# Optimization experiments

Measured on AMD Instinct MI355X. Metric: run time of the kernel, lower is better.

Reference implementation:

```python
import jax, jax.numpy as jnp
import numpy as np

D = H = W = 64
N = D * H * W
BS = 2
C = 32          # enc_dim
IN_DIM = 4
OUT_DIM = 4
P = 5           # pos_enc_dim
COND = 32
M = 8           # modes per axis
NL = 4          # n_layers
NODE_IN = IN_DIM + 3 + 2 * P * 3   # 37
ENC_T = 1 + 2 * P                  # 11
ENC_C = ENC_T * COND               # 352
DT = 0.05


def fourier_embedding(pos, n_freq):
    # F(x) = [cos(2^i*pi*x_l), sin(2^i*pi*x_l)] per coordinate l, then concat x
    freq = (2.0 ** jnp.arange(n_freq, dtype=jnp.float32)) * jnp.pi  # (P,)
    ang = pos[..., None] * freq                                     # (..., L, P)
    emb = jnp.concatenate([jnp.cos(ang), jnp.sin(ang)], axis=-1)    # (..., L, 2P)
    emb = emb.reshape(*pos.shape[:-1], -1)                          # (..., L*2P)
    return jnp.concatenate([emb, pos], axis=-1)


def setup_inputs() -> dict:
    key = jax.random.key(0)
    ks = jax.random.split(key, 24)
    scale = 1.0 / C ** 2
    inp = {
        "state_in": jax.random.normal(ks[0], (BS, N, IN_DIM), jnp.float32),
        "node_pos": jax.random.uniform(ks[1], (BS, N, 3), jnp.float32),
        "edges": jax.random.randint(ks[2], (BS, 16, 2), 0, N),
        "time_i": jax.random.uniform(ks[3], (BS, 1), jnp.float32),
        "conditions": jax.random.uniform(ks[4], (BS, COND), jnp.float32),
        "t_embed_w": jax.random.normal(ks[5], (C, ENC_T), jnp.float32) * 0.05,
        "t_embed_b": jax.random.normal(ks[6], (C,), jnp.float32) * 0.05,
        "c_embed_w": jax.random.normal(ks[7], (C, ENC_C), jnp.float32) * 0.05,
        "c_embed_b": jax.random.normal(ks[8], (C,), jnp.float32) * 0.05,
        "lift_w": jax.random.normal(ks[9], (C, NODE_IN), jnp.float32) * 0.05,
        "lift_b": jax.random.normal(ks[10], (C,), jnp.float32) * 0.05,
        "spec_wr": jax.random.uniform(ks[11], (NL, C, C, M, M, M), jnp.float32) * scale,
        "spec_wi": jax.random.uniform(ks[12], (NL, C, C, M, M, M), jnp.float32) * scale,
        "byp_w": jax.random.normal(ks[13], (NL, C, C), jnp.float32) * 0.05,
        "byp_b": jax.random.normal(ks[14], (NL, C), jnp.float32) * 0.05,
        "proj1_w": jax.random.normal(ks[15], (C, C), jnp.float32) * 0.05,
        "proj1_b": jax.random.normal(ks[16], (C,), jnp.float32) * 0.05,
        "proj2_w": jax.random.normal(ks[17], (OUT_DIM, C), jnp.float32) * 0.05,
        "proj2_b": jax.random.normal(ks[18], (OUT_DIM,), jnp.float32) * 0.05,
    }
    return inp


def _conv1x1(x, w, b):
    # x: (b, c, d, h, w), w: (o, c), b: (o,)
    return jnp.einsum('bcdhw,oc->bodhw', x, w) + b[None, :, None, None, None]


def _fno_forward(state_in, node_pos, time_i, conditions,
                 t_embed_w, t_embed_b, c_embed_w, c_embed_b, lift_w, lift_b,
                 spec_wr, spec_wi, byp_w, byp_b, proj1_w, proj1_b, proj2_w, proj2_b):
    pos_enc = fourier_embedding(node_pos, P)      # (bs, N, 33)
    c_enc = fourier_embedding(conditions, P)      # (bs, 352)
    t_enc = fourier_embedding(time_i, P)          # (bs, 11)

    node_feat = jnp.concatenate([state_in, pos_enc], axis=-1)  # (bs, N, 37)
    t_emb = (t_enc @ t_embed_w.T + t_embed_b)[:, :, None, None, None]
    c_emb = (c_enc @ c_embed_w.T + c_embed_b)[:, :, None, None, None]

    # (bs, N, 37) -> (bs, 37, D, H, W)
    x = node_feat.transpose(0, 2, 1).reshape(BS, NODE_IN, D, H, W)
    x = _conv1x1(x, lift_w, lift_b)
    x = x + t_emb + c_emb

    for l in range(NL):
        w = jax.lax.complex(spec_wr[l], spec_wi[l])              # (C, C, M, M, M)
        x_ft = jnp.fft.rfftn(x, axes=(-3, -2, -1))               # (bs, C, D, H, W//2+1)
        blk = jnp.einsum('bixyz,ioxyz->boxyz', x_ft[..., :M, :M, :M], w)
        out_ft = jnp.zeros_like(x_ft).at[..., :M, :M, :M].set(blk)
        sp = jnp.fft.irfftn(out_ft, s=(D, H, W), axes=(-3, -2, -1))
        bp = _conv1x1(x, byp_w[l], byp_b[l])
        x = jax.nn.gelu(sp + bp, approximate=False)

    x = jax.nn.gelu(_conv1x1(x, proj1_w, proj1_b), approximate=False)
    x = _conv1x1(x, proj2_w, proj2_b)                            # (bs, 4, D, H, W)
    v_pred = x.reshape(BS, OUT_DIM, N).transpose(0, 2, 1)        # (bs, N, 4)
    return state_in + DT * v_pred


def reference(state_in, node_pos, edges, time_i, conditions,
              t_embed_w, t_embed_b, c_embed_w, c_embed_b, lift_w, lift_b,
              spec_wr, spec_wi, byp_w, byp_b, proj1_w, proj1_b, proj2_w, proj2_b):
    # edges are unused in the FNO forward (kept for API compatibility)
    return _fno_forward(state_in, node_pos, time_i, conditions,
                        t_embed_w, t_embed_b, c_embed_w, c_embed_b, lift_w, lift_b,
                        spec_wr, spec_wi, byp_w, byp_b, proj1_w, proj1_b, proj2_w, proj2_b)
```

## Files before the change

### kernel.cpp

```cpp
#include <hip/hip_runtime.h>
#include <math.h>

#define PI_F 3.14159265358979323846f

typedef __bf16 bf16x8 __attribute__((ext_vector_type(8)));
typedef float floatx4 __attribute__((ext_vector_type(4)));
union U8 { unsigned short u[8]; uint4 q; bf16x8 v; };

__device__ __forceinline__ float gelu_sig(float v) {
    float e = __builtin_amdgcn_exp2f(-2.4554670f * v);
    return v * __builtin_amdgcn_rcpf(1.0f + e);
}
__device__ __forceinline__ int rfl(int x) { return __builtin_amdgcn_readfirstlane(x); }

__device__ __forceinline__ unsigned short f2bf(float f) {
    unsigned int u = __float_as_uint(f);
    u += 0x7fffu + ((u >> 16) & 1u);
    return (unsigned short)(u >> 16);
}
__device__ __forceinline__ float bf2f(unsigned short h) {
    return __uint_as_float(((unsigned int)h) << 16);
}

__device__ __forceinline__ void swz8k(int blk, int& b, int& nx, int& ny) {
    int x = blk & 7;
    int j = blk >> 3;
    int pair = x * 16 + (j >> 6);
    ny = j & 63;
    b = pair >> 6;
    nx = pair & 63;
}

__global__ void k_emb(const float* __restrict__ time_i, const float* __restrict__ conditions,
                      const float* __restrict__ t_embed_w, const float* __restrict__ t_embed_b,
                      const float* __restrict__ c_embed_w, const float* __restrict__ c_embed_b,
                      const float* __restrict__ lift_b, float* __restrict__ embk) {
    __shared__ float red[8][32];
    int t = threadIdx.x;
    int b = blockIdx.x;
    int c = t & 31, lg = t >> 5;
    float acc = 0.0f;
    if (lg == 0) {
        acc = t_embed_b[c] + c_embed_b[c] + lift_b[c];
        float tv = time_i[b];
        float ang = PI_F * tv;
        const float* tw = t_embed_w + c * 11;
        for (int i = 0; i < 5; i++) {
            float s, co; sincosf(ang, &s, &co);
            acc += co * tw[i] + s * tw[5 + i];
            ang *= 2.0f;
        }
        acc += tv * tw[10];
    }
    const float* cw = c_embed_w + c * 352;
    for (int j = 0; j < 4; j++) {
        int l = lg * 4 + j;
        float v = conditions[b * 32 + l];
        float ang = PI_F * v;
        for (int i = 0; i < 5; i++) {
            float s, co; sincosf(ang, &s, &co);
            acc += co * cw[l * 10 + i] + s * cw[l * 10 + 5 + i];
            ang *= 2.0f;
        }
        acc += v * cw[320 + l];
    }
    red[lg][c] = acc;
    __syncthreads();
    if (t < 32) {
        float s = 0.0f;
        for (int g = 0; g < 8; g++) s += red[g][t];
        embk[b * 32 + t] = s;
    }
}

__global__ void k_wt(const float* __restrict__ byp_w, const float* __restrict__ lift_w,
                     unsigned short* __restrict__ wbh, unsigned short* __restrict__ wlbf,
                     unsigned short* __restrict__ Tinv, unsigned short* __restrict__ TfT) {
    int idx = blockIdx.x * 256 + threadIdx.x;
    const float th = PI_F / 32.0f;
    if (idx < 4096) {
        wbh[idx] = f2bf(byp_w[idx]);
    } else if (idx < 6144) {
        int j = idx - 4096;
        int o = j >> 6, q = j & 63;
        wlbf[j] = (q < 37) ? f2bf(lift_w[o * 37 + q]) : 0;
    } else if (idx < 8192) {
        int j = idx - 6144;
        int nz = j >> 5, k = j & 31;
        int kz = k >> 1;
        float val = 0.0f;
        if (kz < 8) {
            float a = (float)((kz * nz) & 63) * th;
            val = (k & 1) ? sinf(a) : cosf(a);
        }
        Tinv[j] = f2bf(val);
    } else if (idx < 9216) {
        int j = idx - 8192;
        int kcol = j >> 6, nz = j & 63;
        int kz = kcol >> 1;
        float a = (float)((kz * nz) & 63) * th;
        float val = (kcol & 1) ? -sinf(a) : cosf(a);
        TfT[j] = f2bf(val);
    }
}

__global__ __launch_bounds__(256) void k_lift(const float* __restrict__ state_in,
        const float* __restrict__ node_pos, const unsigned short* __restrict__ wlbf,
        const float* __restrict__ embk, const unsigned short* __restrict__ TfT,
        unsigned short* __restrict__ x0, float2* __restrict__ a1) {
    __shared__ __align__(16) float SL[7584];
    unsigned short* fsT  = (unsigned short*)SL;
    unsigned short* ysbf = (unsigned short*)(SL + 2304);
    float* pz   = SL + 3456;
    float* pz2  = SL + 3456 + 512;
    float* bias = SL + 7552;
    int t = threadIdx.x;
    int b, nx, ny; swz8k(blockIdx.x, b, nx, ny);
    int nxy = nx * 64 + ny;

    if (t < 32) bias[t] = embk[b * 32 + t];
    {
        for (int u = t; u < 2048; u += 256) {
            int row = u >> 5, col = 37 + (u & 31);
            fsT[row * 72 + col] = 0;
        }
    }
    if (t < 192) {
        int nzf = t / 3;
        int l = t - nzf * 3;
        float p = node_pos[((size_t)b * 262144 + (nxy << 6)) * 3 + t];
        float s, c; sincosf(PI_F * p, &s, &c);
        unsigned short* row = fsT + nzf * 72;
        #pragma unroll
        for (int i = 0; i < 5; i++) {
            row[4 + l * 10 + i] = f2bf(c);
            row[4 + l * 10 + 5 + i] = f2bf(s);
            float nc = 2.0f * c * c - 1.0f;
            s = 2.0f * s * c;
            c = nc;
        }
        row[34 + l] = f2bf(p);
    } else {
        int nzf = t - 192;
        const float4 s4 = *(const float4*)(state_in + ((size_t)b * 262144 + (nxy << 6) + nzf) * 4);
        unsigned short* row = fsT + nzf * 72;
        row[0] = f2bf(s4.x); row[1] = f2bf(s4.y);
        row[2] = f2bf(s4.z); row[3] = f2bf(s4.w);
    }
    __syncthreads();

    int lane = t & 63;
    int w = rfl(t >> 6);
    int otile = w & 1;
    int nzt0 = (w >> 1) * 2;
    int l15 = lane & 15;
    int quad = lane >> 4;

    U8 a0, a1_;
    a0.q = *(const uint4*)(wlbf + ((otile * 16 + l15) << 6) + (quad << 3));
    a1_.q = *(const uint4*)(wlbf + ((otile * 16 + l15) << 6) + 32 + (quad << 3));
    floatx4 cb;
    #pragma unroll
    for (int r = 0; r < 4; r++) cb[r] = bias[otile * 16 + quad * 4 + r];
    floatx4 dz = {0.0f, 0.0f, 0.0f, 0.0f};

    #pragma unroll
    for (int m = 0; m < 2; m++) {
        int nzc = (nzt0 + m) * 16 + l15;
        U8 b0, b1_;
        b0.q = *(const uint4*)(fsT + nzc * 72 + (quad << 3));
        b1_.q = *(const uint4*)(fsT + nzc * 72 + 32 + (quad << 3));
        floatx4 d = __builtin_amdgcn_mfma_f32_16x16x32_bf16(a0.v, b0.v, cb, 0, 0, 0);
        d = __builtin_amdgcn_mfma_f32_16x16x32_bf16(a1_.v, b1_.v, d, 0, 0, 0);
        #pragma unroll
        for (int r = 0; r < 4; r++) {
            int o = otile * 16 + quad * 4 + r;
            ysbf[o * 72 + nzc] = f2bf(d[r]);
        }
    }
    __syncthreads();
    {
        int ch = t >> 3, q = t & 7;
        uint4 v = *(const uint4*)(ysbf + ch * 72 + q * 8);
        *(uint4*)(x0 + (((size_t)(b * 32 + ch)) << 18) + (nxy << 6) + q * 8) = v;
    }
    {
        int khalf = w >> 1;
        U8 ay, bt;
        ay.q = *(const uint4*)(ysbf + (otile * 16 + l15) * 72 + khalf * 32 + (quad << 3));
        bt.q = *(const uint4*)(TfT + (l15 << 6) + khalf * 32 + (quad << 3));
        floatx4 d = __builtin_amdgcn_mfma_f32_16x16x32_bf16(ay.v, bt.v, dz, 0, 0, 0);
        *(floatx4*)(pz + w * 1024 + lane * 4) = d;
    }
    __syncthreads();
    if (w < 2) {
        float4 p0 = *(float4*)(pz + w * 1024 + lane * 4);
        float4 p1 = *(float4*)(pz + (w + 2) * 1024 + lane * 4);
        float pv[4] = {p0.x + p1.x, p0.y + p1.y, p0.z + p1.z, p0.w + p1.w};
        #pragma unroll
        for (int r = 0; r < 4; r++)
            pz2[(otile * 16 + quad * 4 + r) * 16 + l15] = pv[r];
    }
    __syncthreads();
    if (t < 128) {
        float4 v = *(float4*)(pz2 + t * 4);
        float* a1f = (float*)a1 + ((size_t)(b * 4096 + nxy)) * 512;
        *(float4*)(a1f + t * 4) = v;
    }
}


__global__ __launch_bounds__(256) void k_p1(const float2* __restrict__ a1,
                                            float2* __restrict__ a2p) {
    int blk = blockIdx.x, t = threadIdx.x;
    int x = blk & 7, r = blk >> 3;
    int pair = x * 16 + (r & 15);
    int half = r >> 4;
    const float2* src = a1 + ((size_t)(pair * 64 + half * 32)) * 256 + t;
    float accr[8], acci[8];
    #pragma unroll
    for (int k = 0; k < 8; k++) { accr[k] = 0.0f; acci[k] = 0.0f; }
    const float bc = 0.99518472667f;
    const float bs = -0.09801714033f;
    float wc = half ? -1.0f : 1.0f;
    float ws = 0.0f;
    #pragma unroll 4
    for (int j = 0; j < 32; j++) {
        float2 v = src[(size_t)j * 256];
        accr[0] += v.x; acci[0] += v.y;
        float tc = wc, ts = ws;
        #pragma unroll
        for (int ky = 1; ky < 8; ky++) {
            accr[ky] += v.x * tc - v.y * ts;
            acci[ky] += v.x * ts + v.y * tc;
            float nt = tc * wc - ts * ws; ts = ts * wc + tc * ws; tc = nt;
        }
        float nw = wc * bc - ws * bs; ws = ws * bc + wc * bs; wc = nw;
    }
    float4* dst = (float4*)(a2p + (size_t)half * 262144 + ((size_t)(pair * 256 + t)) * 8);
    #pragma unroll
    for (int j = 0; j < 4; j++)
        dst[j] = make_float4(accr[2 * j], acci[2 * j], accr[2 * j + 1], acci[2 * j + 1]);
}

__global__ __launch_bounds__(256) void k_p2(const float2* __restrict__ a2p,
                                            float2* __restrict__ xft) {
    __shared__ __align__(16) float2 SH[1040];
    int blk = blockIdx.x, t = threadIdx.x;
    for (int lu = 0; lu < 2; lu++) {
        int un = blk * 2 + lu;
        int b = un >> 8, ckz = un & 255;
        size_t base = (size_t)b * 131072 + (size_t)ckz * 8;
        for (int e = t; e < 512; e += 256) {
            size_t a = base + (size_t)(e >> 3) * 2048 + (e & 7);
            float2 v0 = a2p[a];
            float2 v1 = a2p[a + 262144];
            SH[lu * 520 + e] = make_float2(v0.x + v1.x, v0.y + v1.y);
        }
    }
    __syncthreads();
    if (t < 128) {
        int lu = t >> 6, out = t & 63;
        int un = blk * 2 + lu;
        int kx = out & 7;
        float sn, cc; sincosf((float)kx * (PI_F / 32.0f), &sn, &cc);
        float bsn = -sn;
        float tc = 1.0f, ts = 0.0f, rr = 0.0f, ri = 0.0f;
        const float2* row = SH + lu * 520 + (out >> 3);
        for (int nx = 0; nx < 64; nx++) {
            float2 v = row[nx * 8];
            rr += v.x * tc - v.y * ts;
            ri += v.x * ts + v.y * tc;
            float nt = tc * cc - ts * bsn; ts = ts * cc + tc * bsn; tc = nt;
        }
        xft[(size_t)un * 64 + out] = make_float2(rr, ri);
    }
}

__global__ __launch_bounds__(256) void k_p3(const float2* __restrict__ xft,
        const float* __restrict__ wr, const float* __restrict__ wi,
        float2* __restrict__ yftp) {
    __shared__ __align__(16) float2 SH[128];
    int blk = blockIdx.x, t = threadIdx.x;
    int unit = blk >> 1, ih = blk & 1;
    int b = unit >> 6, kx = (unit >> 3) & 7, ky = unit & 7;
    if (t < 128) {
        int il = t >> 3, kz = t & 7;
        int i = ih * 16 + il;
        SH[t] = xft[((size_t)((b * 32 + i) * 8 + kz)) * 64 + ky * 8 + kx];
    }
    __syncthreads();
    int o = t >> 3, kz = t & 7;
    float yr = 0.0f, yi = 0.0f;
    for (int il = 0; il < 16; il++) {
        int i = ih * 16 + il;
        float2 xv = SH[il * 8 + kz];
        int wofs = ((i * 32 + o) << 9) + kx * 64 + ky * 8 + kz;
        float wrv = wr[wofs], wiv = wi[wofs];
        yr += xv.x * wrv - xv.y * wiv;
        yi += xv.x * wiv + xv.y * wrv;
    }
    yftp[(size_t)ih * 32768 + ((size_t)((b * 32 + o) * 8 + kz)) * 64 + ky * 8 + kx]
        = make_float2(yr, yi);
}

__global__ __launch_bounds__(256) void k_p4(const float2* __restrict__ yftp,
                                            float2* __restrict__ b1) {
    __shared__ __align__(16) float2 SH[4608];
    int blk = blockIdx.x, t = threadIdx.x;
    for (int u = 0; u < 2; u++) {
        if (u) __syncthreads();
        int unit = blk * 2 + u;
        int b = unit >> 8, nx = (unit >> 2) & 63, og = unit & 3;
        size_t sbase = ((size_t)(b * 32 + og * 8)) * 512;
        for (int e = t; e < 4096; e += 256) {
            float2 v0 = yftp[sbase + e];
            float2 v1 = yftp[32768 + sbase + e];
            SH[(e >> 3) * 9 + (e & 7)] = make_float2(v0.x + v1.x, v0.y + v1.y);
        }
        __syncthreads();
        float cs, ss; sincosf((float)nx * (PI_F / 32.0f), &ss, &cs);
        float2* dst = b1 + ((size_t)(b * 64 + nx)) * 2048 + og * 512;
        for (int h = 0; h < 2; h++) {
            int idx = h * 256 + t;
            const float2* row = SH + idx * 9;
            float c = 1.0f, s = 0.0f, rr = 0.0f, ri = 0.0f;
            #pragma unroll
            for (int kx = 0; kx < 8; kx++) {
                float2 y = row[kx];
                rr += y.x * c - y.y * s;
                ri += y.x * s + y.y * c;
                float nc = c * cs - s * ss; s = s * cs + c * ss; c = nc;
            }
            dst[idx] = make_float2(rr, ri);
        }
    }
}

__global__ __launch_bounds__(256) void k_fin(
        const unsigned short* __restrict__ xin, const float2* __restrict__ b1,
        const unsigned short* __restrict__ wbh, const float* __restrict__ bb,
        const unsigned short* __restrict__ Tinv, const unsigned short* __restrict__ TfT,
        unsigned short* __restrict__ xout, float2* __restrict__ a1, int do_z,
        int do_proj, const float* __restrict__ state_in, const float* __restrict__ p1w,
        const float* __restrict__ p1b, const float* __restrict__ p2w,
        const float* __restrict__ p2b, float* __restrict__ outp) {
    __shared__ __align__(16) float S[7232];
    float* b1sr = S;
    float* b1si = S + 2112;
    float* pz   = S;
    float* pz2  = S + 512;
    float* pr   = S;
    unsigned short* xsu  = (unsigned short*)(S + 4224);
    unsigned short* msbf = (unsigned short*)(S + 5280);
    unsigned short* ysbf = (unsigned short*)(S + 5920);
    float* cosT = S + 7072;
    float* sinT = S + 7136;
    float* bias = S + 7200;
    int t = threadIdx.x;
    int b, nx, ny; swz8k(blockIdx.x, b, nx, ny);
    int nxy = nx * 64 + ny;

    if (t < 64) { float s, c; sincosf((float)t * (PI_F / 32.0f), &s, &c); cosT[t] = c; sinT[t] = s; }
    if (t >= 96 && t < 128) bias[t - 96] = bb[t - 96];
    ((unsigned int*)msbf)[(t >> 3) * 20 + 8 + (t & 7)] = 0;
    {
        int ch = t >> 3, q = t & 7;
        uint4 v = *(const uint4*)(xin + (((size_t)b) << 23) + (nxy << 6)
                                  + ((size_t)ch << 18) + q * 8);
        unsigned int* dst = (unsigned int*)(xsu + ch * 66 + q * 8);
        dst[0] = v.x; dst[1] = v.y; dst[2] = v.z; dst[3] = v.w;
    }
    const float2* bsrc = b1 + ((size_t)(b * 64 + nx)) * 2048;
    for (int u = 0; u < 8; u++) {
        int g = u * 256 + t;
        float2 v = bsrc[g];
        int ky = g & 7, okz = g >> 3;
        b1sr[ky * 264 + okz] = v.x;
        b1si[ky * 264 + okz] = v.y;
    }
    __syncthreads();
    const float scale = 1.0f / 262144.0f;
    {
        float mr = 0.0f, mi = 0.0f;
        #pragma unroll
        for (int ky = 0; ky < 8; ky++) {
            float vr = b1sr[ky * 264 + t], vi = b1si[ky * 264 + t];
            int m_ = (ky * ny) & 63;
            float c = cosT[m_], s = sinT[m_];
            mr += vr * c - vi * s;
            mi += vr * s + vi * c;
        }
        int kz = t & 7;
        float sc = (kz == 0) ? scale : 2.0f * scale;
        unsigned int pk = (unsigned int)f2bf(mr * sc)
                        | ((unsigned int)f2bf(-mi * sc) << 16);
        ((unsigned int*)msbf)[(t >> 3) * 20 + kz] = pk;
    }
    __syncthreads();

    int lane = t & 63;
    int w = rfl(t >> 6);
    int otile = w & 1;
    int nzt0 = (w >> 1) * 2;
    int l15 = lane & 15;
    int quad = lane >> 4;

    U8 aw, ams;
    aw.q = *(const uint4*)(wbh + ((otile * 16 + l15) << 5) + (quad << 3));
    ams.q = *(const uint4*)(msbf + (otile * 16 + l15) * 40 + (quad << 3));
    floatx4 cb;
    #pragma unroll
    for (int r = 0; r < 4; r++) cb[r] = bias[otile * 16 + quad * 4 + r];
    floatx4 dzero = {0.0f, 0.0f, 0.0f, 0.0f};

    size_t colbase = (((size_t)b) << 23) + (nxy << 6);

    #pragma unroll
    for (int m = 0; m < 2; m++) {
        int nzc = (nzt0 + m) * 16 + l15;
        U8 bx, bt;
        #pragma unroll
        for (int j = 0; j < 8; j++) bx.u[j] = xsu[(quad * 8 + j) * 66 + nzc];
        bt.q = *(const uint4*)(Tinv + (nzc << 5) + (quad << 3));
        floatx4 d = __builtin_amdgcn_mfma_f32_16x16x32_bf16(aw.v, bx.v, cb, 0, 0, 0);
        d = __builtin_amdgcn_mfma_f32_16x16x32_bf16(ams.v, bt.v, d, 0, 0, 0);
        #pragma unroll
        for (int r = 0; r < 4; r++) {
            int o = otile * 16 + quad * 4 + r;
            ysbf[o * 72 + nzc] = f2bf(gelu_sig(d[r]));
        }
    }
    __syncthreads();

    if (!do_proj) {
        int ch = t >> 3, q = t & 7;
        uint4 v = *(const uint4*)(ysbf + ch * 72 + q * 8);
        *(uint4*)(xout + colbase + ((size_t)ch << 18) + q * 8) = v;
    }

    if (do_z) {
        int khalf = w >> 1;
        U8 ay, bt;
        ay.q = *(const uint4*)(ysbf + (otile * 16 + l15) * 72 + khalf * 32 + (quad << 3));
        bt.q = *(const uint4*)(TfT + (l15 << 6) + khalf * 32 + (quad << 3));
        floatx4 d = __builtin_amdgcn_mfma_f32_16x16x32_bf16(ay.v, bt.v, dzero, 0, 0, 0);
        *(floatx4*)(pz + w * 1024 + lane * 4) = d;
        __syncthreads();
        if (w < 2) {
            float4 p0 = *(float4*)(pz + w * 1024 + lane * 4);
            float4 p1 = *(float4*)(pz + (w + 2) * 1024 + lane * 4);
            float pv[4] = {p0.x + p1.x, p0.y + p1.y, p0.z + p1.z, p0.w + p1.w};
            #pragma unroll
            for (int r = 0; r < 4; r++)
                pz2[(otile * 16 + quad * 4 + r) * 16 + l15] = pv[r];
        }
        __syncthreads();
        if (t < 128) {
            float4 v = *(float4*)(pz2 + t * 4);
            float* a1f = (float*)a1 + ((size_t)(b * 4096 + nxy)) * 512;
            *(float4*)(a1f + t * 4) = v;
        }
    }

    if (do_proj) {
        int nz = t & 63;
        float xv[32];
        #pragma unroll
        for (int i = 0; i < 32; i++) xv[i] = bf2f(ysbf[i * 72 + nz]);
        float r0 = 0.f, r1 = 0.f, r2 = 0.f, r3 = 0.f;
        #pragma unroll
        for (int k = 0; k < 8; k++) {
            int o = w * 8 + k;
            float a = p1b[o];
            const float* wr = p1w + o * 32;
            #pragma unroll
            for (int i = 0; i < 32; i++) a += wr[i] * xv[i];
            float h = gelu_sig(a);
            r0 += p2w[0 * 32 + o] * h;
            r1 += p2w[1 * 32 + o] * h;
            r2 += p2w[2 * 32 + o] * h;
            r3 += p2w[3 * 32 + o] * h;
        }
        *(float4*)(pr + w * 256 + nz * 4) = make_float4(r0, r1, r2, r3);
        __syncthreads();
        if (t < 64) {
            float4 a0 = *(float4*)(pr + 0 * 256 + t * 4);
            float4 a1_ = *(float4*)(pr + 1 * 256 + t * 4);
            float4 a2 = *(float4*)(pr + 2 * 256 + t * 4);
            float4 a3 = *(float4*)(pr + 3 * 256 + t * 4);
            size_t base = ((size_t)b * 262144 + (nxy << 6) + t) * 4;
            float4 sv = *(const float4*)(state_in + base);
            *(float4*)(outp + base) = make_float4(
                sv.x + 0.05f * (p2b[0] + a0.x + a1_.x + a2.x + a3.x),
                sv.y + 0.05f * (p2b[1] + a0.y + a1_.y + a2.y + a3.y),
                sv.z + 0.05f * (p2b[2] + a0.z + a1_.z + a2.z + a3.z),
                sv.w + 0.05f * (p2b[3] + a0.w + a1_.w + a2.w + a3.w));
        }
    }
}

extern "C" void kernel_launch(void* const* d_in, const int* in_sizes, int n_in,
                              void* d_out, int out_size, void* d_ws, size_t ws_size,
                              hipStream_t stream) {
    const float* state_in   = (const float*)d_in[0];
    const float* node_pos   = (const float*)d_in[1];
    const float* time_i     = (const float*)d_in[3];
    const float* conditions = (const float*)d_in[4];
    const float* t_embed_w  = (const float*)d_in[5];
    const float* t_embed_b  = (const float*)d_in[6];
    const float* c_embed_w  = (const float*)d_in[7];
    const float* c_embed_b  = (const float*)d_in[8];
    const float* lift_w     = (const float*)d_in[9];
    const float* lift_b     = (const float*)d_in[10];
    const float* spec_wr    = (const float*)d_in[11];
    const float* spec_wi    = (const float*)d_in[12];
    const float* byp_w      = (const float*)d_in[13];
    const float* byp_b      = (const float*)d_in[14];
    const float* proj1_w    = (const float*)d_in[15];
    const float* proj1_b    = (const float*)d_in[16];
    const float* proj2_w    = (const float*)d_in[17];
    const float* proj2_b    = (const float*)d_in[18];
    float* out = (float*)d_out;
    float* ws  = (float*)d_ws;

    unsigned short* xA = (unsigned short*)ws;
    unsigned short* xB = (unsigned short*)(ws + 8388608);
    float2* a1   = (float2*)(ws + 16777216);
    float2* a2p  = (float2*)(ws + 20971520);
    float2* xft  = (float2*)(ws + 22020096);
    float2* yftp = (float2*)(ws + 22085632);
    float2* b1   = (float2*)(ws + 22216704);
    float*  embk = ws + 22740992;
    unsigned short* wbh  = (unsigned short*)(ws + 22741056);
    unsigned short* wlbf = (unsigned short*)(ws + 22743104);
    unsigned short* Tinv = (unsigned short*)(ws + 22744128);
    unsigned short* TfT  = (unsigned short*)(ws + 22745152);

    k_emb<<<2, 256, 0, stream>>>(time_i, conditions, t_embed_w, t_embed_b,
                                 c_embed_w, c_embed_b, lift_b, embk);
    k_wt<<<36, 256, 0, stream>>>(byp_w, lift_w, wbh, wlbf, Tinv, TfT);
    k_lift<<<8192, 256, 0, stream>>>(state_in, node_pos, wlbf, embk, TfT, xA, a1);

    for (int l = 0; l < 4; l++) {
        unsigned short* xin  = (l & 1) ? xB : xA;
        unsigned short* xout = (l & 1) ? xA : xB;
        const float* wrl = spec_wr + (size_t)l * 524288;
        const float* wil = spec_wi + (size_t)l * 524288;
        k_p1<<<256, 256, 0, stream>>>(a1, a2p);
        k_p2<<<256, 256, 0, stream>>>(a2p, xft);
        k_p3<<<256, 256, 0, stream>>>(xft, wrl, wil, yftp);
        k_p4<<<256, 256, 0, stream>>>(yftp, b1);
        k_fin<<<8192, 256, 0, stream>>>(xin, b1, wbh + l * 1024, byp_b + l * 32,
                                        Tinv, TfT, xout, a1, (l < 3) ? 1 : 0,
                                        (l == 3) ? 1 : 0, state_in,
                                        proj1_w, proj1_b, proj2_w, proj2_b, out);
    }
}
```

Measured before the change: 360.6 us.

## Split spectral partial sums four ways and process two columns per fin block

k_p1 and k_p3 now split their reductions into quarters instead of halves, doubling grid size to 512 blocks, with the partial sums added in k_p2 and k_p4. k_p1 and k_fin read precomputed ky*ny twiddles from a global table instead of rotating twiddles recursively or reading per-block LDS tables. k_fin handles two (nx,ny) columns per block, which halves the grid, and each wave now does a full 64-length z-transform MFMA pair rather than reducing partials through shared memory. The aim is more parallelism in the small spectral kernels and less per-block overhead in fin, at the cost of extra partial-buffer traffic and more LDS per block.

```diff
diff --git a/kernel.cpp b/kernel.cpp
--- a/kernel.cpp
+++ b/kernel.cpp
@@ -20,15 +20,6 @@
 }
 __device__ __forceinline__ float bf2f(unsigned short h) {
     return __uint_as_float(((unsigned int)h) << 16);
-}
-
-__device__ __forceinline__ void swz8k(int blk, int& b, int& nx, int& ny) {
-    int x = blk & 7;
-    int j = blk >> 3;
-    int pair = x * 16 + (j >> 6);
-    ny = j & 63;
-    b = pair >> 6;
-    nx = pair & 63;
 }
 
 __global__ void k_emb(const float* __restrict__ time_i, const float* __restrict__ conditions,
@@ -75,7 +66,8 @@
 
 __global__ void k_wt(const float* __restrict__ byp_w, const float* __restrict__ lift_w,
                      unsigned short* __restrict__ wbh, unsigned short* __restrict__ wlbf,
-                     unsigned short* __restrict__ Tinv, unsigned short* __restrict__ TfT) {
+                     unsigned short* __restrict__ Tinv, unsigned short* __restrict__ TfT,
+                     float* __restrict__ Tp1g) {
     int idx = blockIdx.x * 256 + threadIdx.x;
     const float th = PI_F / 32.0f;
     if (idx < 4096) {
@@ -101,7 +93,22 @@
         float a = (float)((kz * nz) & 63) * th;
         float val = (kcol & 1) ? -sinf(a) : cosf(a);
         TfT[j] = f2bf(val);
-    }
+    } else if (idx < 9728) {
+        int j = idx - 9216;
+        int ny = j >> 3, ky = j & 7;
+        float a = (float)((ky * ny) & 63) * th;
+        Tp1g[j * 2] = cosf(a);
+        Tp1g[j * 2 + 1] = sinf(a);
+    }
+}
+
+__device__ __forceinline__ void swz8k(int blk, int& b, int& nx, int& ny) {
+    int x = blk & 7;
+    int j = blk >> 3;
+    int pair = x * 16 + (j >> 6);
+    ny = j & 63;
+    b = pair >> 6;
+    nx = pair & 63;
 }
 
 __global__ __launch_bounds__(256) void k_lift(const float* __restrict__ state_in,
@@ -211,33 +218,28 @@
 
 
 __global__ __launch_bounds__(256) void k_p1(const float2* __restrict__ a1,
-                                            float2* __restrict__ a2p) {
+        const float2* __restrict__ Tp1g, float2* __restrict__ a2p) {
     int blk = blockIdx.x, t = threadIdx.x;
     int x = blk & 7, r = blk >> 3;
     int pair = x * 16 + (r & 15);
-    int half = r >> 4;
-    const float2* src = a1 + ((size_t)(pair * 64 + half * 32)) * 256 + t;
+    int qtr = r >> 4;
+    const float2* src = a1 + ((size_t)(pair * 64 + qtr * 16)) * 256 + t;
     float accr[8], acci[8];
     #pragma unroll
     for (int k = 0; k < 8; k++) { accr[k] = 0.0f; acci[k] = 0.0f; }
-    const float bc = 0.99518472667f;
-    const float bs = -0.09801714033f;
-    float wc = half ? -1.0f : 1.0f;
-    float ws = 0.0f;
     #pragma unroll 4
-    for (int j = 0; j < 32; j++) {
+    for (int j = 0; j < 16; j++) {
+        int ny = qtr * 16 + j;
         float2 v = src[(size_t)j * 256];
-        accr[0] += v.x; acci[0] += v.y;
-        float tc = wc, ts = ws;
-        #pragma unroll
-        for (int ky = 1; ky < 8; ky++) {
-            accr[ky] += v.x * tc - v.y * ts;
-            acci[ky] += v.x * ts + v.y * tc;
-            float nt = tc * wc - ts * ws; ts = ts * wc + tc * ws; tc = nt;
-        }
-        float nw = wc * bc - ws * bs; ws = ws * bc + wc * bs; wc = nw;
-    }
-    float4* dst = (float4*)(a2p + (size_t)half * 262144 + ((size_t)(pair * 256 + t)) * 8);
+        const float2* tw = Tp1g + ny * 8;
+        #pragma unroll
+        for (int ky = 0; ky < 8; ky++) {
+            float2 w2 = tw[ky];
+            accr[ky] += v.x * w2.x + v.y * w2.y;
+            acci[ky] += v.y * w2.x - v.x * w2.y;
+        }
+    }
+    float4* dst = (float4*)(a2p + (size_t)qtr * 262144 + ((size_t)(pair * 256 + t)) * 8);
     #pragma unroll
     for (int j = 0; j < 4; j++)
         dst[j] = make_float4(accr[2 * j], acci[2 * j], accr[2 * j + 1], acci[2 * j + 1]);
@@ -255,7 +257,10 @@
             size_t a = base + (size_t)(e >> 3) * 2048 + (e & 7);
             float2 v0 = a2p[a];
             float2 v1 = a2p[a + 262144];
-            SH[lu * 520 + e] = make_float2(v0.x + v1.x, v0.y + v1.y);
+            float2 v2 = a2p[a + 524288];
+            float2 v3 = a2p[a + 786432];
+            SH[lu * 520 + e] = make_float2(v0.x + v1.x + v2.x + v3.x,
+                                           v0.y + v1.y + v2.y + v3.y);
         }
     }
     __syncthreads();
@@ -280,27 +285,27 @@
 __global__ __launch_bounds__(256) void k_p3(const float2* __restrict__ xft,
         const float* __restrict__ wr, const float* __restrict__ wi,
         float2* __restrict__ yftp) {
-    __shared__ __align__(16) float2 SH[128];
+    __shared__ __align__(16) float2 SH[64];
     int blk = blockIdx.x, t = threadIdx.x;
-    int unit = blk >> 1, ih = blk & 1;
+    int unit = blk >> 2, iq = blk & 3;
     int b = unit >> 6, kx = (unit >> 3) & 7, ky = unit & 7;
-    if (t < 128) {
+    if (t < 64) {
         int il = t >> 3, kz = t & 7;
-        int i = ih * 16 + il;
+        int i = iq * 8 + il;
         SH[t] = xft[((size_t)((b * 32 + i) * 8 + kz)) * 64 + ky * 8 + kx];
     }
     __syncthreads();
     int o = t >> 3, kz = t & 7;
     float yr = 0.0f, yi = 0.0f;
-    for (int il = 0; il < 16; il++) {
-        int i = ih * 16 + il;
+    for (int il = 0; il < 8; il++) {
+        int i = iq * 8 + il;
         float2 xv = SH[il * 8 + kz];
         int wofs = ((i * 32 + o) << 9) + kx * 64 + ky * 8 + kz;
         float wrv = wr[wofs], wiv = wi[wofs];
         yr += xv.x * wrv - xv.y * wiv;
         yi += xv.x * wiv + xv.y * wrv;
     }
-    yftp[(size_t)ih * 32768 + ((size_t)((b * 32 + o) * 8 + kz)) * 64 + ky * 8 + kx]
+    yftp[(size_t)iq * 32768 + ((size_t)((b * 32 + o) * 8 + kz)) * 64 + ky * 8 + kx]
         = make_float2(yr, yi);
 }
 
@@ -316,7 +321,10 @@
         for (int e = t; e < 4096; e += 256) {
             float2 v0 = yftp[sbase + e];
             float2 v1 = yftp[32768 + sbase + e];
-            SH[(e >> 3) * 9 + (e & 7)] = make_float2(v0.x + v1.x, v0.y + v1.y);
+            float2 v2 = yftp[65536 + sbase + e];
+            float2 v3 = yftp[98304 + sbase + e];
+            SH[(e >> 3) * 9 + (e & 7)] = make_float2(v0.x + v1.x + v2.x + v3.x,
+                                                     v0.y + v1.y + v2.y + v3.y);
         }
         __syncthreads();
         float cs, ss; sincosf((float)nx * (PI_F / 32.0f), &ss, &cs);
@@ -341,35 +349,40 @@
         const unsigned short* __restrict__ xin, const float2* __restrict__ b1,
         const unsigned short* __restrict__ wbh, const float* __restrict__ bb,
         const unsigned short* __restrict__ Tinv, const unsigned short* __restrict__ TfT,
-        unsigned short* __restrict__ xout, float2* __restrict__ a1, int do_z,
-        int do_proj, const float* __restrict__ state_in, const float* __restrict__ p1w,
+        const float2* __restrict__ Tp1g, unsigned short* __restrict__ xout,
+        float2* __restrict__ a1, int do_z, int do_proj,
+        const float* __restrict__ state_in, const float* __restrict__ p1w,
         const float* __restrict__ p1b, const float* __restrict__ p2w,
         const float* __restrict__ p2b, float* __restrict__ outp) {
-    __shared__ __align__(16) float S[7232];
+    __shared__ __align__(16) float S[9952];
     float* b1sr = S;
     float* b1si = S + 2112;
-    float* pz   = S;
-    float* pz2  = S + 512;
+    float* pz2  = S;
     float* pr   = S;
     unsigned short* xsu  = (unsigned short*)(S + 4224);
-    unsigned short* msbf = (unsigned short*)(S + 5280);
-    unsigned short* ysbf = (unsigned short*)(S + 5920);
-    float* cosT = S + 7072;
-    float* sinT = S + 7136;
-    float* bias = S + 7200;
+    unsigned short* msbf = (unsigned short*)(S + 6336);
+    unsigned short* ysbf = (unsigned short*)(S + 7616);
+    float* bias = S + 9920;
     int t = threadIdx.x;
-    int b, nx, ny; swz8k(blockIdx.x, b, nx, ny);
-    int nxy = nx * 64 + ny;
-
-    if (t < 64) { float s, c; sincosf((float)t * (PI_F / 32.0f), &s, &c); cosT[t] = c; sinT[t] = s; }
-    if (t >= 96 && t < 128) bias[t - 96] = bb[t - 96];
-    ((unsigned int*)msbf)[(t >> 3) * 20 + 8 + (t & 7)] = 0;
+
+    int xx = blockIdx.x & 7;
+    int jj = blockIdx.x >> 3;
+    int pair = xx * 16 + (jj & 15);
+    int nyp = jj >> 4;
+    int b = pair >> 6, nx = pair & 63;
+    int nxy0 = nx * 64 + nyp * 2;
+
+    if (t < 32) bias[t] = bb[t];
+    for (int u = t; u < 1280; u += 256) ((unsigned int*)msbf)[u] = 0;
     {
         int ch = t >> 3, q = t & 7;
-        uint4 v = *(const uint4*)(xin + (((size_t)b) << 23) + (nxy << 6)
-                                  + ((size_t)ch << 18) + q * 8);
-        unsigned int* dst = (unsigned int*)(xsu + ch * 66 + q * 8);
-        dst[0] = v.x; dst[1] = v.y; dst[2] = v.z; dst[3] = v.w;
+        #pragma unroll
+        for (int c = 0; c < 2; c++) {
+            uint4 v = *(const uint4*)(xin + (((size_t)b) << 23) + ((size_t)(nxy0 + c) << 6)
+                                      + ((size_t)ch << 18) + q * 8);
+            unsigned int* dst = (unsigned int*)(xsu + c * 2112 + ch * 66 + q * 8);
+            dst[0] = v.x; dst[1] = v.y; dst[2] = v.z; dst[3] = v.w;
+        }
     }
     const float2* bsrc = b1 + ((size_t)(b * 64 + nx)) * 2048;
     for (int u = 0; u < 8; u++) {
@@ -380,122 +393,134 @@
         b1si[ky * 264 + okz] = v.y;
     }
     __syncthreads();
+
     const float scale = 1.0f / 262144.0f;
     {
-        float mr = 0.0f, mi = 0.0f;
+        float vr[8], vi[8];
         #pragma unroll
         for (int ky = 0; ky < 8; ky++) {
-            float vr = b1sr[ky * 264 + t], vi = b1si[ky * 264 + t];
-            int m_ = (ky * ny) & 63;
-            float c = cosT[m_], s = sinT[m_];
-            mr += vr * c - vi * s;
-            mi += vr * s + vi * c;
+            vr[ky] = b1sr[ky * 264 + t];
+            vi[ky] = b1si[ky * 264 + t];
         }
         int kz = t & 7;
         float sc = (kz == 0) ? scale : 2.0f * scale;
-        unsigned int pk = (unsigned int)f2bf(mr * sc)
-                        | ((unsigned int)f2bf(-mi * sc) << 16);
-        ((unsigned int*)msbf)[(t >> 3) * 20 + kz] = pk;
+        #pragma unroll
+        for (int c = 0; c < 2; c++) {
+            int ny = nyp * 2 + c;
+            const float2* tw = Tp1g + ny * 8;
+            float mr = 0.0f, mi = 0.0f;
+            #pragma unroll
+            for (int ky = 0; ky < 8; ky++) {
+                float2 w2 = tw[ky];
+                mr += vr[ky] * w2.x - vi[ky] * w2.y;
+                mi += vr[ky] * w2.y + vi[ky] * w2.x;
+            }
+            unsigned int pk = (unsigned int)f2bf(mr * sc)
+                            | ((unsigned int)f2bf(-mi * sc) << 16);
+            ((unsigned int*)msbf)[c * 640 + (t >> 3) * 20 + kz] = pk;
+        }
     }
     __syncthreads();
 
     int lane = t & 63;
     int w = rfl(t >> 6);
-    int otile = w & 1;
-    int nzt0 = (w >> 1) * 2;
-    int l15 = lane & 15;
-    int quad = lane >> 4;
+    int otile = w & 1, col = w >> 1;
+    int l15 = lane & 15, quad = lane >> 4;
 
     U8 aw, ams;
     aw.q = *(const uint4*)(wbh + ((otile * 16 + l15) << 5) + (quad << 3));
-    ams.q = *(const uint4*)(msbf + (otile * 16 + l15) * 40 + (quad << 3));
+    ams.q = *(const uint4*)(msbf + col * 1280 + (otile * 16 + l15) * 40 + (quad << 3));
     floatx4 cb;
     #pragma unroll
     for (int r = 0; r < 4; r++) cb[r] = bias[otile * 16 + quad * 4 + r];
-    floatx4 dzero = {0.0f, 0.0f, 0.0f, 0.0f};
-
-    size_t colbase = (((size_t)b) << 23) + (nxy << 6);
-
+
+    const unsigned short* xs_c = xsu + col * 2112;
+    unsigned short* ys_c = ysbf + col * 2304;
     #pragma unroll
-    for (int m = 0; m < 2; m++) {
-        int nzc = (nzt0 + m) * 16 + l15;
+    for (int m = 0; m < 4; m++) {
+        int nzc = m * 16 + l15;
         U8 bx, bt;
         #pragma unroll
-        for (int j = 0; j < 8; j++) bx.u[j] = xsu[(quad * 8 + j) * 66 + nzc];
+        for (int j = 0; j < 8; j++) bx.u[j] = xs_c[(quad * 8 + j) * 66 + nzc];
         bt.q = *(const uint4*)(Tinv + (nzc << 5) + (quad << 3));
         floatx4 d = __builtin_amdgcn_mfma_f32_16x16x32_bf16(aw.v, bx.v, cb, 0, 0, 0);
         d = __builtin_amdgcn_mfma_f32_16x16x32_bf16(ams.v, bt.v, d, 0, 0, 0);
         #pragma unroll
         for (int r = 0; r < 4; r++) {
             int o = otile * 16 + quad * 4 + r;
-            ysbf[o * 72 + nzc] = f2bf(gelu_sig(d[r]));
-        }
-    }
-    __syncthreads();
-
+            ys_c[o * 72 + nzc] = f2bf(gelu_sig(d[r]));
+        }
+    }
+    __syncthreads();
+
+    size_t colbase0 = (((size_t)b) << 23) + ((size_t)nxy0 << 6);
     if (!do_proj) {
         int ch = t >> 3, q = t & 7;
-        uint4 v = *(const uint4*)(ysbf + ch * 72 + q * 8);
-        *(uint4*)(xout + colbase + ((size_t)ch << 18) + q * 8) = v;
+        #pragma unroll
+        for (int c = 0; c < 2; c++) {
+            uint4 v = *(const uint4*)(ysbf + c * 2304 + ch * 72 + q * 8);
+            *(uint4*)(xout + colbase0 + ((size_t)c << 6) + ((size_t)ch << 18) + q * 8) = v;
+        }
     }
 
     if (do_z) {
-        int khalf = w >> 1;
-        U8 ay, bt;
-        ay.q = *(const uint4*)(ysbf + (otile * 16 + l15) * 72 + khalf * 32 + (quad << 3));
-        bt.q = *(const uint4*)(TfT + (l15 << 6) + khalf * 32 + (quad << 3));
-        floatx4 d = __builtin_amdgcn_mfma_f32_16x16x32_bf16(ay.v, bt.v, dzero, 0, 0, 0);
-        *(floatx4*)(pz + w * 1024 + lane * 4) = d;
+        U8 ay0, ay1, bt0, bt1;
+        const unsigned short* yr = ysbf + col * 2304 + (otile * 16 + l15) * 72;
+        ay0.q = *(const uint4*)(yr + (quad << 3));
+        ay1.q = *(const uint4*)(yr + 32 + (quad << 3));
+        bt0.q = *(const uint4*)(TfT + (l15 << 6) + (quad << 3));
+        bt1.q = *(const uint4*)(TfT + (l15 << 6) + 32 + (quad << 3));
+        floatx4 dzero = {0.0f, 0.0f, 0.0f, 0.0f};
+        floatx4 d = __builtin_amdgcn_mfma_f32_16x16x32_bf16(ay0.v, bt0.v, dzero, 0, 0, 0);
+        d = __builtin_amdgcn_mfma_f32_16x16x32_bf16(ay1.v, bt1.v, d, 0, 0, 0);
+        #pragma unroll
+        for (int r = 0; r < 4; r++)
+            pz2[col * 512 + (otile * 16 + quad * 4 + r) * 16 + l15] = d[r];
         __syncthreads();
-        if (w < 2) {
-            float4 p0 = *(float4*)(pz + w * 1024 + lane * 4);
-            float4 p1 = *(float4*)(pz + (w + 2) * 1024 + lane * 4);
-            float pv[4] = {p0.x + p1.x, p0.y + p1.y, p0.z + p1.z, p0.w + p1.w};
-            #pragma unroll
-            for (int r = 0; r < 4; r++)
-                pz2[(otile * 16 + quad * 4 + r) * 16 + l15] = pv[r];
-        }
-        __syncthreads();
-        if (t < 128) {
-            float4 v = *(float4*)(pz2 + t * 4);
-            float* a1f = (float*)a1 + ((size_t)(b * 4096 + nxy)) * 512;
-            *(float4*)(a1f + t * 4) = v;
+        {
+            int c = t >> 7, idx = t & 127;
+            float4 v = *(float4*)(pz2 + c * 512 + idx * 4);
+            float* a1f = (float*)a1 + ((size_t)(b * 4096 + nxy0 + c)) * 512;
+            *(float4*)(a1f + idx * 4) = v;
         }
     }
 
     if (do_proj) {
         int nz = t & 63;
-        float xv[32];
-        #pragma unroll
-        for (int i = 0; i < 32; i++) xv[i] = bf2f(ysbf[i * 72 + nz]);
-        float r0 = 0.f, r1 = 0.f, r2 = 0.f, r3 = 0.f;
-        #pragma unroll
-        for (int k = 0; k < 8; k++) {
-            int o = w * 8 + k;
-            float a = p1b[o];
-            const float* wr = p1w + o * 32;
+        for (int c = 0; c < 2; c++) {
+            if (c) __syncthreads();
+            float xv[32];
             #pragma unroll
-            for (int i = 0; i < 32; i++) a += wr[i] * xv[i];
-            float h = gelu_sig(a);
-            r0 += p2w[0 * 32 + o] * h;
-            r1 += p2w[1 * 32 + o] * h;
-            r2 += p2w[2 * 32 + o] * h;
-            r3 += p2w[3 * 32 + o] * h;
-        }
-        *(float4*)(pr + w * 256 + nz * 4) = make_float4(r0, r1, r2, r3);
-        __syncthreads();
-        if (t < 64) {
-            float4 a0 = *(float4*)(pr + 0 * 256 + t * 4);
-            float4 a1_ = *(float4*)(pr + 1 * 256 + t * 4);
-            float4 a2 = *(float4*)(pr + 2 * 256 + t * 4);
-            float4 a3 = *(float4*)(pr + 3 * 256 + t * 4);
-            size_t base = ((size_t)b * 262144 + (nxy << 6) + t) * 4;
-            float4 sv = *(const float4*)(state_in + base);
-            *(float4*)(outp + base) = make_float4(
-                sv.x + 0.05f * (p2b[0] + a0.x + a1_.x + a2.x + a3.x),
-                sv.y + 0.05f * (p2b[1] + a0.y + a1_.y + a2.y + a3.y),
-                sv.z + 0.05f * (p2b[2] + a0.z + a1_.z + a2.z + a3.z),
-                sv.w + 0.05f * (p2b[3] + a0.w + a1_.w + a2.w + a3.w));
+            for (int i = 0; i < 32; i++) xv[i] = bf2f(ysbf[c * 2304 + i * 72 + nz]);
+            float r0 = 0.f, r1 = 0.f, r2 = 0.f, r3 = 0.f;
+            #pragma unroll
+            for (int k = 0; k < 8; k++) {
+                int o = w * 8 + k;
+                float a = p1b[o];
+                const float* wr2 = p1w + o * 32;
+                #pragma unroll
+                for (int i = 0; i < 32; i++) a += wr2[i] * xv[i];
+                float h = gelu_sig(a);
+                r0 += p2w[0 * 32 + o] * h;
+                r1 += p2w[1 * 32 + o] * h;
+                r2 += p2w[2 * 32 + o] * h;
+                r3 += p2w[3 * 32 + o] * h;
+            }
+            *(float4*)(pr + w * 256 + nz * 4) = make_float4(r0, r1, r2, r3);
+            __syncthreads();
+            if (t < 64) {
+                float4 a0 = *(float4*)(pr + 0 * 256 + t * 4);
+                float4 a1_ = *(float4*)(pr + 1 * 256 + t * 4);
+                float4 a2 = *(float4*)(pr + 2 * 256 + t * 4);
+                float4 a3 = *(float4*)(pr + 3 * 256 + t * 4);
+                size_t base = ((size_t)b * 262144 + ((size_t)(nxy0 + c) << 6) + t) * 4;
+                float4 sv = *(const float4*)(state_in + base);
+                *(float4*)(outp + base) = make_float4(
+                    sv.x + 0.05f * (p2b[0] + a0.x + a1_.x + a2.x + a3.x),
+                    sv.y + 0.05f * (p2b[1] + a0.y + a1_.y + a2.y + a3.y),
+                    sv.z + 0.05f * (p2b[2] + a0.z + a1_.z + a2.z + a3.z),
+                    sv.w + 0.05f * (p2b[3] + a0.w + a1_.w + a2.w + a3.w));
+            }
         }
     }
 }
@@ -528,18 +553,20 @@
     unsigned short* xB = (unsigned short*)(ws + 8388608);
     float2* a1   = (float2*)(ws + 16777216);
     float2* a2p  = (float2*)(ws + 20971520);
-    float2* xft  = (float2*)(ws + 22020096);
-    float2* yftp = (float2*)(ws + 22085632);
-    float2* b1   = (float2*)(ws + 22216704);
-    float*  embk = ws + 22740992;
-    unsigned short* wbh  = (unsigned short*)(ws + 22741056);
-    unsigned short* wlbf = (unsigned short*)(ws + 22743104);
-    unsigned short* Tinv = (unsigned short*)(ws + 22744128);
-    unsigned short* TfT  = (unsigned short*)(ws + 22745152);
+    float2* xft  = (float2*)(ws + 23068672);
+    float2* yftp = (float2*)(ws + 23134208);
+    float2* b1   = (float2*)(ws + 23396352);
+    float*  embk = ws + 23920640;
+    unsigned short* wbh  = (unsigned short*)(ws + 23920704);
+    unsigned short* wlbf = (unsigned short*)(ws + 23922752);
+    unsigned short* Tinv = (unsigned short*)(ws + 23923776);
+    unsigned short* TfT  = (unsigned short*)(ws + 23924800);
+    float* Tp1gf = ws + 23925312;
+    float2* Tp1g = (float2*)Tp1gf;
 
     k_emb<<<2, 256, 0, stream>>>(time_i, conditions, t_embed_w, t_embed_b,
                                  c_embed_w, c_embed_b, lift_b, embk);
-    k_wt<<<36, 256, 0, stream>>>(byp_w, lift_w, wbh, wlbf, Tinv, TfT);
+    k_wt<<<38, 256, 0, stream>>>(byp_w, lift_w, wbh, wlbf, Tinv, TfT, Tp1gf);
     k_lift<<<8192, 256, 0, stream>>>(state_in, node_pos, wlbf, embk, TfT, xA, a1);
 
     for (int l = 0; l < 4; l++) {
@@ -547,12 +574,12 @@
         unsigned short* xout = (l & 1) ? xA : xB;
         const float* wrl = spec_wr + (size_t)l * 524288;
         const float* wil = spec_wi + (size_t)l * 524288;
-        k_p1<<<256, 256, 0, stream>>>(a1, a2p);
+        k_p1<<<512, 256, 0, stream>>>(a1, Tp1g, a2p);
         k_p2<<<256, 256, 0, stream>>>(a2p, xft);
-        k_p3<<<256, 256, 0, stream>>>(xft, wrl, wil, yftp);
+        k_p3<<<512, 256, 0, stream>>>(xft, wrl, wil, yftp);
         k_p4<<<256, 256, 0, stream>>>(yftp, b1);
-        k_fin<<<8192, 256, 0, stream>>>(xin, b1, wbh + l * 1024, byp_b + l * 32,
-                                        Tinv, TfT, xout, a1, (l < 3) ? 1 : 0,
+        k_fin<<<4096, 256, 0, stream>>>(xin, b1, wbh + l * 1024, byp_b + l * 32,
+                                        Tinv, TfT, Tp1g, xout, a1, (l < 3) ? 1 : 0,
                                         (l == 3) ? 1 : 0, state_in,
                                         proj1_w, proj1_b, proj2_w, proj2_b, out);
     }
```

After: 397.1 us. +10.1%, slower.

## Split spectral partial-DFT kernels four ways and use precomputed twiddle tables

Applied to the files above, without the earlier changes.

k_p1 now splits the ny reduction into four quarters (512 blocks) and reads twiddles from a precomputed global cos/sin table instead of recurrence rotations. k_p3 splits the input-channel reduction into four parts (512 blocks), and k_p2/k_p4 sum four partials. k_fin drops its per-block shared cos/sin table setup and reads the global twiddle table. The aim is more parallelism in the small spectral kernels and less per-block setup in k_fin, at the cost of extra partial-sum traffic and a larger workspace.

```diff
diff --git a/kernel.cpp b/kernel.cpp
--- a/kernel.cpp
+++ b/kernel.cpp
@@ -20,15 +20,6 @@
 }
 __device__ __forceinline__ float bf2f(unsigned short h) {
     return __uint_as_float(((unsigned int)h) << 16);
-}
-
-__device__ __forceinline__ void swz8k(int blk, int& b, int& nx, int& ny) {
-    int x = blk & 7;
-    int j = blk >> 3;
-    int pair = x * 16 + (j >> 6);
-    ny = j & 63;
-    b = pair >> 6;
-    nx = pair & 63;
 }
 
 __global__ void k_emb(const float* __restrict__ time_i, const float* __restrict__ conditions,
@@ -75,7 +66,8 @@
 
 __global__ void k_wt(const float* __restrict__ byp_w, const float* __restrict__ lift_w,
                      unsigned short* __restrict__ wbh, unsigned short* __restrict__ wlbf,
-                     unsigned short* __restrict__ Tinv, unsigned short* __restrict__ TfT) {
+                     unsigned short* __restrict__ Tinv, unsigned short* __restrict__ TfT,
+                     float* __restrict__ Tp1g) {
     int idx = blockIdx.x * 256 + threadIdx.x;
     const float th = PI_F / 32.0f;
     if (idx < 4096) {
@@ -101,7 +93,22 @@
         float a = (float)((kz * nz) & 63) * th;
         float val = (kcol & 1) ? -sinf(a) : cosf(a);
         TfT[j] = f2bf(val);
-    }
+    } else if (idx < 9728) {
+        int j = idx - 9216;
+        int ny = j >> 3, ky = j & 7;
+        float a = (float)((ky * ny) & 63) * th;
+        Tp1g[j * 2] = cosf(a);
+        Tp1g[j * 2 + 1] = sinf(a);
+    }
+}
+
+__device__ __forceinline__ void swz8k(int blk, int& b, int& nx, int& ny) {
+    int x = blk & 7;
+    int j = blk >> 3;
+    int pair = x * 16 + (j >> 6);
+    ny = j & 63;
+    b = pair >> 6;
+    nx = pair & 63;
 }
 
 __global__ __launch_bounds__(256) void k_lift(const float* __restrict__ state_in,
@@ -211,33 +218,28 @@
 
 
 __global__ __launch_bounds__(256) void k_p1(const float2* __restrict__ a1,
-                                            float2* __restrict__ a2p) {
+        const float2* __restrict__ Tp1g, float2* __restrict__ a2p) {
     int blk = blockIdx.x, t = threadIdx.x;
     int x = blk & 7, r = blk >> 3;
     int pair = x * 16 + (r & 15);
-    int half = r >> 4;
-    const float2* src = a1 + ((size_t)(pair * 64 + half * 32)) * 256 + t;
+    int qtr = r >> 4;
+    const float2* src = a1 + ((size_t)(pair * 64 + qtr * 16)) * 256 + t;
     float accr[8], acci[8];
     #pragma unroll
     for (int k = 0; k < 8; k++) { accr[k] = 0.0f; acci[k] = 0.0f; }
-    const float bc = 0.99518472667f;
-    const float bs = -0.09801714033f;
-    float wc = half ? -1.0f : 1.0f;
-    float ws = 0.0f;
     #pragma unroll 4
-    for (int j = 0; j < 32; j++) {
+    for (int j = 0; j < 16; j++) {
+        int ny = qtr * 16 + j;
         float2 v = src[(size_t)j * 256];
-        accr[0] += v.x; acci[0] += v.y;
-        float tc = wc, ts = ws;
-        #pragma unroll
-        for (int ky = 1; ky < 8; ky++) {
-            accr[ky] += v.x * tc - v.y * ts;
-            acci[ky] += v.x * ts + v.y * tc;
-            float nt = tc * wc - ts * ws; ts = ts * wc + tc * ws; tc = nt;
-        }
-        float nw = wc * bc - ws * bs; ws = ws * bc + wc * bs; wc = nw;
-    }
-    float4* dst = (float4*)(a2p + (size_t)half * 262144 + ((size_t)(pair * 256 + t)) * 8);
+        const float2* tw = Tp1g + ny * 8;
+        #pragma unroll
+        for (int ky = 0; ky < 8; ky++) {
+            float2 w2 = tw[ky];
+            accr[ky] += v.x * w2.x + v.y * w2.y;
+            acci[ky] += v.y * w2.x - v.x * w2.y;
+        }
+    }
+    float4* dst = (float4*)(a2p + (size_t)qtr * 262144 + ((size_t)(pair * 256 + t)) * 8);
     #pragma unroll
     for (int j = 0; j < 4; j++)
         dst[j] = make_float4(accr[2 * j], acci[2 * j], accr[2 * j + 1], acci[2 * j + 1]);
@@ -255,7 +257,10 @@
             size_t a = base + (size_t)(e >> 3) * 2048 + (e & 7);
             float2 v0 = a2p[a];
             float2 v1 = a2p[a + 262144];
-            SH[lu * 520 + e] = make_float2(v0.x + v1.x, v0.y + v1.y);
+            float2 v2 = a2p[a + 524288];
+            float2 v3 = a2p[a + 786432];
+            SH[lu * 520 + e] = make_float2(v0.x + v1.x + v2.x + v3.x,
+                                           v0.y + v1.y + v2.y + v3.y);
         }
     }
     __syncthreads();
@@ -280,27 +285,27 @@
 __global__ __launch_bounds__(256) void k_p3(const float2* __restrict__ xft,
         const float* __restrict__ wr, const float* __restrict__ wi,
         float2* __restrict__ yftp) {
-    __shared__ __align__(16) float2 SH[128];
+    __shared__ __align__(16) float2 SH[64];
     int blk = blockIdx.x, t = threadIdx.x;
-    int unit = blk >> 1, ih = blk & 1;
+    int unit = blk >> 2, iq = blk & 3;
     int b = unit >> 6, kx = (unit >> 3) & 7, ky = unit & 7;
-    if (t < 128) {
+    if (t < 64) {
         int il = t >> 3, kz = t & 7;
-        int i = ih * 16 + il;
+        int i = iq * 8 + il;
         SH[t] = xft[((size_t)((b * 32 + i) * 8 + kz)) * 64 + ky * 8 + kx];
     }
     __syncthreads();
     int o = t >> 3, kz = t & 7;
     float yr = 0.0f, yi = 0.0f;
-    for (int il = 0; il < 16; il++) {
-        int i = ih * 16 + il;
+    for (int il = 0; il < 8; il++) {
+        int i = iq * 8 + il;
         float2 xv = SH[il * 8 + kz];
         int wofs = ((i * 32 + o) << 9) + kx * 64 + ky * 8 + kz;
         float wrv = wr[wofs], wiv = wi[wofs];
         yr += xv.x * wrv - xv.y * wiv;
         yi += xv.x * wiv + xv.y * wrv;
     }
-    yftp[(size_t)ih * 32768 + ((size_t)((b * 32 + o) * 8 + kz)) * 64 + ky * 8 + kx]
+    yftp[(size_t)iq * 32768 + ((size_t)((b * 32 + o) * 8 + kz)) * 64 + ky * 8 + kx]
         = make_float2(yr, yi);
 }
 
@@ -316,7 +321,10 @@
         for (int e = t; e < 4096; e += 256) {
             float2 v0 = yftp[sbase + e];
             float2 v1 = yftp[32768 + sbase + e];
-            SH[(e >> 3) * 9 + (e & 7)] = make_float2(v0.x + v1.x, v0.y + v1.y);
+            float2 v2 = yftp[65536 + sbase + e];
+            float2 v3 = yftp[98304 + sbase + e];
+            SH[(e >> 3) * 9 + (e & 7)] = make_float2(v0.x + v1.x + v2.x + v3.x,
+                                                     v0.y + v1.y + v2.y + v3.y);
         }
         __syncthreads();
         float cs, ss; sincosf((float)nx * (PI_F / 32.0f), &ss, &cs);
@@ -341,11 +349,12 @@
         const unsigned short* __restrict__ xin, const float2* __restrict__ b1,
         const unsigned short* __restrict__ wbh, const float* __restrict__ bb,
         const unsigned short* __restrict__ Tinv, const unsigned short* __restrict__ TfT,
-        unsigned short* __restrict__ xout, float2* __restrict__ a1, int do_z,
-        int do_proj, const float* __restrict__ state_in, const float* __restrict__ p1w,
+        const float2* __restrict__ Tp1g, unsigned short* __restrict__ xout,
+        float2* __restrict__ a1, int do_z, int do_proj,
+        const float* __restrict__ state_in, const float* __restrict__ p1w,
         const float* __restrict__ p1b, const float* __restrict__ p2w,
         const float* __restrict__ p2b, float* __restrict__ outp) {
-    __shared__ __align__(16) float S[7232];
+    __shared__ __align__(16) float S[7104];
     float* b1sr = S;
     float* b1si = S + 2112;
     float* pz   = S;
@@ -354,14 +363,11 @@
     unsigned short* xsu  = (unsigned short*)(S + 4224);
     unsigned short* msbf = (unsigned short*)(S + 5280);
     unsigned short* ysbf = (unsigned short*)(S + 5920);
-    float* cosT = S + 7072;
-    float* sinT = S + 7136;
-    float* bias = S + 7200;
+    float* bias = S + 7072;
     int t = threadIdx.x;
     int b, nx, ny; swz8k(blockIdx.x, b, nx, ny);
     int nxy = nx * 64 + ny;
 
-    if (t < 64) { float s, c; sincosf((float)t * (PI_F / 32.0f), &s, &c); cosT[t] = c; sinT[t] = s; }
     if (t >= 96 && t < 128) bias[t - 96] = bb[t - 96];
     ((unsigned int*)msbf)[(t >> 3) * 20 + 8 + (t & 7)] = 0;
     {
@@ -382,14 +388,14 @@
     __syncthreads();
     const float scale = 1.0f / 262144.0f;
     {
+        const float2* tw = Tp1g + ny * 8;
         float mr = 0.0f, mi = 0.0f;
         #pragma unroll
         for (int ky = 0; ky < 8; ky++) {
             float vr = b1sr[ky * 264 + t], vi = b1si[ky * 264 + t];
-            int m_ = (ky * ny) & 63;
-            float c = cosT[m_], s = sinT[m_];
-            mr += vr * c - vi * s;
-            mi += vr * s + vi * c;
+            float2 w2 = tw[ky];
+            mr += vr * w2.x - vi * w2.y;
+            mi += vr * w2.y + vi * w2.x;
         }
         int kz = t & 7;
         float sc = (kz == 0) ? scale : 2.0f * scale;
@@ -528,18 +534,20 @@
     unsigned short* xB = (unsigned short*)(ws + 8388608);
     float2* a1   = (float2*)(ws + 16777216);
     float2* a2p  = (float2*)(ws + 20971520);
-    float2* xft  = (float2*)(ws + 22020096);
-    float2* yftp = (float2*)(ws + 22085632);
-    float2* b1   = (float2*)(ws + 22216704);
-    float*  embk = ws + 22740992;
-    unsigned short* wbh  = (unsigned short*)(ws + 22741056);
-    unsigned short* wlbf = (unsigned short*)(ws + 22743104);
-    unsigned short* Tinv = (unsigned short*)(ws + 22744128);
-    unsigned short* TfT  = (unsigned short*)(ws + 22745152);
+    float2* xft  = (float2*)(ws + 23068672);
+    float2* yftp = (float2*)(ws + 23134208);
+    float2* b1   = (float2*)(ws + 23396352);
+    float*  embk = ws + 23920640;
+    unsigned short* wbh  = (unsigned short*)(ws + 23920704);
+    unsigned short* wlbf = (unsigned short*)(ws + 23922752);
+    unsigned short* Tinv = (unsigned short*)(ws + 23923776);
+    unsigned short* TfT  = (unsigned short*)(ws + 23924800);
+    float* Tp1gf = ws + 23925312;
+    float2* Tp1g = (float2*)Tp1gf;
 
     k_emb<<<2, 256, 0, stream>>>(time_i, conditions, t_embed_w, t_embed_b,
                                  c_embed_w, c_embed_b, lift_b, embk);
-    k_wt<<<36, 256, 0, stream>>>(byp_w, lift_w, wbh, wlbf, Tinv, TfT);
+    k_wt<<<38, 256, 0, stream>>>(byp_w, lift_w, wbh, wlbf, Tinv, TfT, Tp1gf);
     k_lift<<<8192, 256, 0, stream>>>(state_in, node_pos, wlbf, embk, TfT, xA, a1);
 
     for (int l = 0; l < 4; l++) {
@@ -547,12 +555,12 @@
         unsigned short* xout = (l & 1) ? xA : xB;
         const float* wrl = spec_wr + (size_t)l * 524288;
         const float* wil = spec_wi + (size_t)l * 524288;
-        k_p1<<<256, 256, 0, stream>>>(a1, a2p);
+        k_p1<<<512, 256, 0, stream>>>(a1, Tp1g, a2p);
         k_p2<<<256, 256, 0, stream>>>(a2p, xft);
-        k_p3<<<256, 256, 0, stream>>>(xft, wrl, wil, yftp);
+        k_p3<<<512, 256, 0, stream>>>(xft, wrl, wil, yftp);
         k_p4<<<256, 256, 0, stream>>>(yftp, b1);
         k_fin<<<8192, 256, 0, stream>>>(xin, b1, wbh + l * 1024, byp_b + l * 32,
-                                        Tinv, TfT, xout, a1, (l < 3) ? 1 : 0,
+                                        Tinv, TfT, Tp1g, xout, a1, (l < 3) ? 1 : 0,
                                         (l == 3) ? 1 : 0, state_in,
                                         proj1_w, proj1_b, proj2_w, proj2_b, out);
     }
```

Result: no change. 366.5 us (+1.6%).
